# Kernel tuning notes

Hardware: AMD Instinct MI355X
Metric: run time of the kernel (lower is better)

## Reference

```python
import jax, jax.numpy as jnp
import numpy as np
import math

D = 512
L = 1024
B = 2
N_SETS = 4
PLANES = 4
POS_PLANES = 16
TOTAL_PLANES = N_SETS * PLANES


def setup_inputs() -> dict:
    key = jax.random.key(0)
    ks = jax.random.split(key, 24)
    s = 0.02
    rn = lambda k, shp: jax.random.normal(k, shp, dtype=jnp.float32) * s
    inp = {
        "x": jax.random.normal(ks[0], (B, L, D), dtype=jnp.float32),
        # key encoder: Linear(D,D) -> GELU -> Linear(D,total_planes)
        "ke_w1": rn(ks[1], (D, D)), "ke_b1": jnp.zeros((D,), jnp.float32),
        "ke_w2": rn(ks[2], (D, TOTAL_PLANES)), "ke_b2": jnp.zeros((TOTAL_PLANES,), jnp.float32),
        # query encoder
        "qe_w1": rn(ks[3], (D, D)), "qe_b1": jnp.zeros((D,), jnp.float32),
        "qe_w2": rn(ks[4], (D, TOTAL_PLANES)), "qe_b2": jnp.zeros((TOTAL_PLANES,), jnp.float32),
        # to_value
        "v_w": rn(ks[5], (D, D)), "v_b": jnp.zeros((D,), jnp.float32),
        # to_out: LayerNorm(D) then Linear(D,D)
        "ln_g": jnp.ones((D,), jnp.float32), "ln_b": jnp.zeros((D,), jnp.float32),
        "out_w": rn(ks[6], (D, D)), "out_b": jnp.zeros((D,), jnp.float32),
        # set mixing weights, positional weight
        "set_weights": jnp.ones((N_SETS,), jnp.float32),
        "pos_weight": jnp.ones((1,), jnp.float32),
        # content_pos_gate: Linear(D, D//2) -> GELU -> Linear(D//2, 1) -> Sigmoid
        "gate_w1": rn(ks[7], (D, D // 2)), "gate_b1": jnp.zeros((D // 2,), jnp.float32),
        "gate_w2": rn(ks[8], (D // 2, 1)), "gate_b2": jnp.zeros((1,), jnp.float32),
        # positional frequencies (buffer)
        "pos_freqs": jnp.exp(jnp.arange(POS_PLANES, dtype=jnp.float32) * (-math.log(10000.0) / POS_PLANES)),
    }
    return inp


def reference(x, ke_w1, ke_b1, ke_w2, ke_b2, qe_w1, qe_b1, qe_w2, qe_b2,
              v_w, v_b, ln_g, ln_b, out_w, out_b, set_weights, pos_weight,
              gate_w1, gate_b1, gate_w2, gate_b2, pos_freqs):
    b, l, d = x.shape
    n_sets = set_weights.shape[0]
    total_planes = ke_w2.shape[1]
    planes = total_planes // n_sets

    gelu = lambda t: jax.nn.gelu(t, approximate=False)  # torch default GELU is exact

    key_phase = jnp.tanh(gelu(x @ ke_w1 + ke_b1) @ ke_w2 + ke_b2) * math.pi  # [B,L,P]
    query_phase = jnp.tanh(gelu(x @ qe_w1 + qe_b1) @ qe_w2 + qe_b2) * math.pi
    V = x @ v_w + v_b  # [B,L,D]

    kp = key_phase.reshape(b, l, n_sets, planes)
    qp = query_phase.reshape(b, l, n_sets, planes)
    w = jax.nn.softmax(set_weights)

    # complex phasor outer-product cumsum in real arithmetic:
    # bound = exp(i*kp) * V ; memory = cumsum_L(bound) ; retrieved = Re(memory * exp(-i*qp))
    Vb = V[:, :, None, None, :]                                   # [B,L,1,1,D]
    cum_re = jnp.cumsum(jnp.cos(kp)[..., None] * Vb, axis=1)      # [B,L,S,p,D]
    cum_im = jnp.cumsum(jnp.sin(kp)[..., None] * Vb, axis=1)
    retrieved = (cum_re * jnp.cos(qp)[..., None] + cum_im * jnp.sin(qp)[..., None]).sum(axis=3)  # [B,L,S,D]
    total_retrieved = jnp.einsum('blsd,s->bld', retrieved, w)

    # positional plane
    pos = jnp.arange(l, dtype=jnp.float32)[:, None]
    pos_phase = pos * pos_freqs * (2.0 * math.pi)                 # [L,PP]
    cp = jnp.cos(pos_phase)[None, :, :, None]                     # [1,L,PP,1]
    sp = jnp.sin(pos_phase)[None, :, :, None]
    Vp = V[:, :, None, :]                                          # [B,L,1,D]
    cumP_re = jnp.cumsum(cp * Vp, axis=1)                          # [B,L,PP,D]
    cumP_im = jnp.cumsum(sp * Vp, axis=1)
    retrieved_pos = (cumP_re * cp + cumP_im * sp).sum(axis=2)      # [B,L,D]

    gate = jax.nn.sigmoid(gelu(x @ gate_w1 + gate_b1) @ gate_w2 + gate_b2)  # [B,L,1]
    pos_contribution = jax.nn.sigmoid(pos_weight) * retrieved_pos
    total_retrieved = gate * total_retrieved + (1.0 - gate) * pos_contribution

    positions = jnp.arange(1, l + 1, dtype=jnp.float32)
    norm = jnp.sqrt(positions * planes)[None, :, None]
    h = total_retrieved / norm

    # to_out: LayerNorm then Linear
    mu = h.mean(axis=-1, keepdims=True)
    var = ((h - mu) ** 2).mean(axis=-1, keepdims=True)
    h_ln = (h - mu) / jnp.sqrt(var + 1e-5) * ln_g + ln_b
    return x + h_ln @ out_w + out_b
```

## Files before the change

kernel.cpp:

```cpp
#include <hip/hip_runtime.h>

typedef unsigned short u16;
typedef __attribute__((ext_vector_type(8))) __bf16 bf16x8;
typedef __attribute__((ext_vector_type(4))) float f32x4;

#define DI __device__ __forceinline__

DI u16 f2b(float f){ union{float f; unsigned u;} x; x.f = f; unsigned u = x.u;
  return (u16)((u + 0x7FFFu + ((u>>16)&1u)) >> 16); }

#define NCH 16
#define CLEN 64

__global__ __launch_bounds__(256) void k_cast(const float* __restrict__ x, u16* __restrict__ xb) {
  int i = (blockIdx.x*256 + threadIdx.x)*8;
  float4 a = *(const float4*)(x+i);
  float4 b = *(const float4*)(x+i+4);
  unsigned o0 = (unsigned)f2b(a.x) | ((unsigned)f2b(a.y)<<16);
  unsigned o1 = (unsigned)f2b(a.z) | ((unsigned)f2b(a.w)<<16);
  unsigned o2 = (unsigned)f2b(b.x) | ((unsigned)f2b(b.y)<<16);
  unsigned o3 = (unsigned)f2b(b.z) | ((unsigned)f2b(b.w)<<16);
  *(uint4*)(xb+i) = make_uint4(o0,o1,o2,o3);
}

__global__ void k_transpose(const float* w0, const float* w1, const float* w2, const float* w3, const float* w4,
                            u16* t0, u16* t1, u16* t2, u16* t3, u16* t4) {
  __shared__ u16 tile[32][33];
  int z = blockIdx.z;
  const float* src; u16* dst; int K, N;
  if (z==0){src=w0;dst=t0;K=512;N=512;}
  else if(z==1){src=w1;dst=t1;K=512;N=512;}
  else if(z==2){src=w2;dst=t2;K=512;N=512;}
  else if(z==3){src=w3;dst=t3;K=512;N=256;}
  else        {src=w4;dst=t4;K=512;N=512;}
  int n0 = blockIdx.x*32, k0 = blockIdx.y*32;
  if (n0 >= N) return;
  int tx = threadIdx.x, ty = threadIdx.y;
  #pragma unroll
  for (int r = 0; r < 4; r++) tile[ty + 8*r][tx] = f2b(src[(k0 + ty + 8*r)*N + n0 + tx]);
  __syncthreads();
  #pragma unroll
  for (int r = 0; r < 4; r++) dst[(n0 + ty + 8*r)*K + k0 + tx] = tile[tx][ty + 8*r];
}

__global__ __launch_bounds__(256) void k_gemm4(const u16* __restrict__ A, const u16* __restrict__ BTF,
                       const float* __restrict__ kb1, const float* __restrict__ qb1,
                       const float* __restrict__ vb,  const float* __restrict__ gb1,
                       float* __restrict__ Hke, float* __restrict__ Hqe,
                       float* __restrict__ V,   float* __restrict__ Hg) {
  const int K = 512;
  __shared__ short As[64][48];
  __shared__ short Bs[64][48];
  int t = threadIdx.x;
  int bm = blockIdx.y*64, bn = blockIdx.x*64;
  int lane = t & 63, wid = t >> 6;
  int wm = (wid>>1)*32, wn = (wid&1)*32;
  int lr = lane & 15, ls = lane >> 4;
  f32x4 zero = {0.f,0.f,0.f,0.f};
  f32x4 acc[2][2];
  acc[0][0]=zero; acc[0][1]=zero; acc[1][0]=zero; acc[1][1]=zero;
  int srow = t >> 2, scol = (t & 3)*8;
  for (int k0 = 0; k0 < K; k0 += 32) {
    __syncthreads();
    *(bf16x8*)&As[srow][scol] = *(const bf16x8*)(A   + (bm+srow)*K + k0 + scol);
    *(bf16x8*)&Bs[srow][scol] = *(const bf16x8*)(BTF + (bn+srow)*K + k0 + scol);
    __syncthreads();
    bf16x8 a0 = *(const bf16x8*)&As[wm + lr][ls*8];
    bf16x8 a1 = *(const bf16x8*)&As[wm + 16 + lr][ls*8];
    bf16x8 b0 = *(const bf16x8*)&Bs[wn + lr][ls*8];
    bf16x8 b1 = *(const bf16x8*)&Bs[wn + 16 + lr][ls*8];
    acc[0][0] = __builtin_amdgcn_mfma_f32_16x16x32_bf16(a0, b0, acc[0][0], 0,0,0);
    acc[0][1] = __builtin_amdgcn_mfma_f32_16x16x32_bf16(a0, b1, acc[0][1], 0,0,0);
    acc[1][0] = __builtin_amdgcn_mfma_f32_16x16x32_bf16(a1, b0, acc[1][0], 0,0,0);
    acc[1][1] = __builtin_amdgcn_mfma_f32_16x16x32_bf16(a1, b1, acc[1][1], 0,0,0);
  }
  float* C; const float* bias; int nstr, nb; bool gel;
  if (bn < 512)       { C=Hke; bias=kb1; nstr=512; nb=bn;      gel=true;  }
  else if (bn < 1024) { C=Hqe; bias=qb1; nstr=512; nb=bn-512;  gel=true;  }
  else if (bn < 1536) { C=V;   bias=vb;  nstr=512; nb=bn-1024; gel=false; }
  else                { C=Hg;  bias=gb1; nstr=256; nb=bn-1536; gel=true;  }
  #pragma unroll
  for (int fm = 0; fm < 2; fm++)
    #pragma unroll
    for (int fn = 0; fn < 2; fn++)
      #pragma unroll
      for (int r = 0; r < 4; r++) {
        int grow = bm + wm + fm*16 + ls*4 + r;
        int gcol = nb + wn + fn*16 + lr;
        float v = acc[fm][fn][r] + bias[gcol];
        if (gel) v = 0.5f*v*(1.0f + erff(v*0.70710678118654752f));
        C[grow*nstr + gcol] = v;
      }
}

__global__ __launch_bounds__(256) void k_gemm_out(const u16* __restrict__ A, const u16* __restrict__ BT,
                       const float* __restrict__ bias, const float* __restrict__ resid,
                       float* __restrict__ C, int M, int N, int K) {
  __shared__ short As[64][48];
  __shared__ short Bs[64][48];
  int t = threadIdx.x;
  int bm = blockIdx.y*64, bn = blockIdx.x*64;
  int lane = t & 63, wid = t >> 6;
  int wm = (wid>>1)*32, wn = (wid&1)*32;
  int lr = lane & 15, ls = lane >> 4;
  f32x4 zero = {0.f,0.f,0.f,0.f};
  f32x4 acc[2][2];
  acc[0][0]=zero; acc[0][1]=zero; acc[1][0]=zero; acc[1][1]=zero;
  int srow = t >> 2, scol = (t & 3)*8;
  for (int k0 = 0; k0 < K; k0 += 32) {
    __syncthreads();
    *(bf16x8*)&As[srow][scol] = *(const bf16x8*)(A  + (bm+srow)*K + k0 + scol);
    *(bf16x8*)&Bs[srow][scol] = *(const bf16x8*)(BT + (bn+srow)*K + k0 + scol);
    __syncthreads();
    bf16x8 a0 = *(const bf16x8*)&As[wm + lr][ls*8];
    bf16x8 a1 = *(const bf16x8*)&As[wm + 16 + lr][ls*8];
    bf16x8 b0 = *(const bf16x8*)&Bs[wn + lr][ls*8];
    bf16x8 b1 = *(const bf16x8*)&Bs[wn + 16 + lr][ls*8];
    acc[0][0] = __builtin_amdgcn_mfma_f32_16x16x32_bf16(a0, b0, acc[0][0], 0,0,0);
    acc[0][1] = __builtin_amdgcn_mfma_f32_16x16x32_bf16(a0, b1, acc[0][1], 0,0,0);
    acc[1][0] = __builtin_amdgcn_mfma_f32_16x16x32_bf16(a1, b0, acc[1][0], 0,0,0);
    acc[1][1] = __builtin_amdgcn_mfma_f32_16x16x32_bf16(a1, b1, acc[1][1], 0,0,0);
  }
  #pragma unroll
  for (int fm = 0; fm < 2; fm++)
    #pragma unroll
    for (int fn = 0; fn < 2; fn++)
      #pragma unroll
      for (int r = 0; r < 4; r++) {
        int grow = bm + wm + fm*16 + ls*4 + r;
        int gcol = bn + wn + fn*16 + lr;
        float v = acc[fm][fn][r] + bias[gcol] + resid[grow*N + gcol];
        C[grow*N + gcol] = v;
      }
}

__global__ __launch_bounds__(256) void k_phase(const float* __restrict__ Hke, const float* __restrict__ Hqe,
                        const float* __restrict__ Hg,
                        const float* __restrict__ kw2, const float* __restrict__ kb2,
                        const float* __restrict__ qw2, const float* __restrict__ qb2,
                        const float* __restrict__ gw2, const float* __restrict__ gb2,
                        const float* __restrict__ setw, const float* __restrict__ posw,
                        const float* __restrict__ freqs,
                        float* __restrict__ ub, float* __restrict__ ab) {
  int t = threadIdx.x;
  int wid = t >> 6, lane = t & 63;
  int r = blockIdx.x*4 + wid;
  int l = r & 1023;
  int p = lane & 15, s = lane >> 4;
  const float* hk = Hke + r*512 + s*128;
  const float* hq = Hqe + r*512 + s*128;
  float kps = 0.f, qps = 0.f;
  for (int i0 = 0; i0 < 128; i0 += 4) {
    float4 hkv = *(const float4*)(hk + i0);
    float4 hqv = *(const float4*)(hq + i0);
    int kb = (s*128 + i0)*16 + p;
    kps += hkv.x * kw2[kb];      qps += hqv.x * qw2[kb];
    kps += hkv.y * kw2[kb+16];   qps += hqv.y * qw2[kb+16];
    kps += hkv.z * kw2[kb+32];   qps += hqv.z * qw2[kb+32];
    kps += hkv.w * kw2[kb+48];   qps += hqv.w * qw2[kb+48];
  }
  kps += __shfl_xor(kps, 16); kps += __shfl_xor(kps, 32);
  qps += __shfl_xor(qps, 16); qps += __shfl_xor(qps, 32);
  const float PI = 3.14159265358979323846f;
  float kph = tanhf(kps + kb2[p]) * PI;
  float qph = tanhf(qps + qb2[p]) * PI;
  const float* hg = Hg + r*256;
  float4 hgv = *(const float4*)(hg + lane*4);
  float gp = hgv.x*gw2[lane*4] + hgv.y*gw2[lane*4+1]
           + hgv.z*gw2[lane*4+2] + hgv.w*gw2[lane*4+3];
  #pragma unroll
  for (int m = 1; m <= 32; m <<= 1) gp += __shfl_xor(gp, m);
  float gate = 1.f/(1.f + expf(-(gp + gb2[0])));
  float pph = (float)l * freqs[p] * 6.2831853071795864769f;
  float s0=setw[0], s1=setw[1], s2=setw[2], s3=setw[3];
  float mx = fmaxf(fmaxf(s0,s1), fmaxf(s2,s3));
  float e0=expf(s0-mx), e1=expf(s1-mx), e2=expf(s2-mx), e3=expf(s3-mx);
  float esum = e0+e1+e2+e3;
  int si = p >> 2;
  float wsel = (si==0? e0 : si==1? e1 : si==2? e2 : e3) / esum;
  float sigpw = 1.f/(1.f + expf(-posw[0]));
  float invnorm = rsqrtf((float)(l+1) * 4.0f);
  if (lane < 16) {
    float sk, ck, sq, cq, sp, cp;
    sincosf(kph, &sk, &ck);
    sincosf(qph, &sq, &cq);
    sincosf(pph, &sp, &cp);
    float* urow = ub + r*64;
    float* arow = ab + r*64;
    urow[p]      = ck;
    urow[16 + p] = sk;
    urow[32 + p] = cp;
    urow[48 + p] = sp;
    float ga = gate * wsel * invnorm;
    float pa = (1.f - gate) * sigpw * invnorm;
    arow[p]      = ga * cq;
    arow[16 + p] = ga * sq;
    arow[32 + p] = pa * cp;
    arow[48 + p] = pa * sp;
  }
}

__global__ __launch_bounds__(256) void k_scanA(const float* __restrict__ ub, const float* __restrict__ V,
                        float* __restrict__ P) {
  __shared__ float ul[CLEN][64];
  __shared__ float vl[CLEN][64];
  int t = threadIdx.x;
  int d0 = blockIdx.x*64; int c = blockIdx.y; int b = blockIdx.z;
  int srow = t >> 2, scol = (t & 3)*16;
  {
    const float* up = ub + (b*1024 + c*CLEN + srow)*64 + scol;
    *(float4*)&ul[srow][scol]    = *(const float4*)up;
    *(float4*)&ul[srow][scol+4]  = *(const float4*)(up+4);
    *(float4*)&ul[srow][scol+8]  = *(const float4*)(up+8);
    *(float4*)&ul[srow][scol+12] = *(const float4*)(up+12);
    const float* vp = V + (b*1024 + c*CLEN + srow)*512 + d0 + scol;
    *(float4*)&vl[srow][scol]    = *(const float4*)vp;
    *(float4*)&vl[srow][scol+4]  = *(const float4*)(vp+4);
    *(float4*)&vl[srow][scol+8]  = *(const float4*)(vp+8);
    *(float4*)&vl[srow][scol+12] = *(const float4*)(vp+12);
  }
  __syncthreads();
  int dd = t & 63, kg = t >> 6;
  float acc[16];
  #pragma unroll
  for (int i=0;i<16;i++) acc[i]=0.f;
  for (int tt = 0; tt < CLEN; tt++) {
    float vv = vl[tt][dd];
    #pragma unroll
    for (int i=0;i<16;i++) acc[i] += ul[tt][kg*16+i]*vv;
  }
  float* pp = P + (((b*NCH + c)*64) + kg*16)*512 + d0 + dd;
  #pragma unroll
  for (int i=0;i<16;i++) pp[i*512] = acc[i];
}

__global__ __launch_bounds__(256) void k_scanB(float* __restrict__ P) {
  int tid = blockIdx.x*256 + threadIdx.x;
  int b = tid >> 15;
  int k = (tid >> 9) & 63;
  int d = tid & 511;
  float run = 0.f;
  float* base = P + ((b*NCH)*64 + k)*512 + d;
  for (int c = 0; c < NCH; c++) {
    float v = base[c*64*512];
    base[c*64*512] = run;
    run += v;
  }
}

__global__ __launch_bounds__(256) void k_scanC(const float* __restrict__ ub, const float* __restrict__ ab,
                        const float* __restrict__ V, const float* __restrict__ P,
                        float* __restrict__ h) {
  __shared__ float ul[CLEN][64];
  __shared__ float al[CLEN][64];
  int t = threadIdx.x;
  int c = blockIdx.y; int b = blockIdx.z;
  int srow = t >> 2, scol = (t & 3)*16;
  {
    const float* up = ub + (b*1024 + c*CLEN + srow)*64 + scol;
    *(float4*)&ul[srow][scol]    = *(const float4*)up;
    *(float4*)&ul[srow][scol+4]  = *(const float4*)(up+4);
    *(float4*)&ul[srow][scol+8]  = *(const float4*)(up+8);
    *(float4*)&ul[srow][scol+12] = *(const float4*)(up+12);
    const float* ap = ab + (b*1024 + c*CLEN + srow)*64 + scol;
    *(float4*)&al[srow][scol]    = *(const float4*)ap;
    *(float4*)&al[srow][scol+4]  = *(const float4*)(ap+4);
    *(float4*)&al[srow][scol+8]  = *(const float4*)(ap+8);
    *(float4*)&al[srow][scol+12] = *(const float4*)(ap+12);
  }
  __syncthreads();
  int kg = t & 3;
  int di = t >> 2;
  int d = blockIdx.x*64 + di;
  float s[16];
  const float* pb = P + ((b*NCH + c)*64 + kg*16)*512 + d;
  #pragma unroll
  for (int k = 0; k < 16; k++) s[k] = pb[k*512];
  const float* vrow = V + (b*1024 + c*CLEN)*512 + d;
  float* hrow = h + (b*1024 + c*CLEN)*512 + d;
  const float4* ul4 = (const float4*)&ul[0][0];
  const float4* al4 = (const float4*)&al[0][0];
  for (int tt = 0; tt < CLEN; tt++) {
    float vv = vrow[tt*512];
    float4 u0 = ul4[tt*16 + kg*4 + 0];
    float4 u1 = ul4[tt*16 + kg*4 + 1];
    float4 u2 = ul4[tt*16 + kg*4 + 2];
    float4 u3 = ul4[tt*16 + kg*4 + 3];
    float4 a0 = al4[tt*16 + kg*4 + 0];
    float4 a1 = al4[tt*16 + kg*4 + 1];
    float4 a2 = al4[tt*16 + kg*4 + 2];
    float4 a3 = al4[tt*16 + kg*4 + 3];
    float h0=0.f, h1=0.f, h2=0.f, h3=0.f;
    s[0]  += u0.x*vv; h0 += a0.x*s[0];
    s[1]  += u0.y*vv; h1 += a0.y*s[1];
    s[2]  += u0.z*vv; h2 += a0.z*s[2];
    s[3]  += u0.w*vv; h3 += a0.w*s[3];
    s[4]  += u1.x*vv; h0 += a1.x*s[4];
    s[5]  += u1.y*vv; h1 += a1.y*s[5];
    s[6]  += u1.z*vv; h2 += a1.z*s[6];
    s[7]  += u1.w*vv; h3 += a1.w*s[7];
    s[8]  += u2.x*vv; h0 += a2.x*s[8];
    s[9]  += u2.y*vv; h1 += a2.y*s[9];
    s[10] += u2.z*vv; h2 += a2.z*s[10];
    s[11] += u2.w*vv; h3 += a2.w*s[11];
    s[12] += u3.x*vv; h0 += a3.x*s[12];
    s[13] += u3.y*vv; h1 += a3.y*s[13];
    s[14] += u3.z*vv; h2 += a3.z*s[14];
    s[15] += u3.w*vv; h3 += a3.w*s[15];
    float hp = (h0+h1)+(h2+h3);
    hp += __shfl_xor(hp, 1);
    hp += __shfl_xor(hp, 2);
    if (kg == 0) hrow[tt*512] = hp;
  }
}

__global__ __launch_bounds__(256) void k_ln(const float* __restrict__ h, const float* __restrict__ g,
                     const float* __restrict__ bta, u16* __restrict__ hln) {
  int t = threadIdx.x;
  int wid = t >> 6, lane = t & 63;
  int r = blockIdx.x*4 + wid;
  const float* hr = h + r*512;
  float4 v0 = *(const float4*)(hr + lane*8);
  float4 v1 = *(const float4*)(hr + lane*8 + 4);
  float vals[8] = {v0.x,v0.y,v0.z,v0.w,v1.x,v1.y,v1.z,v1.w};
  float sum = 0.f, sq = 0.f;
  #pragma unroll
  for (int i=0;i<8;i++){ sum += vals[i]; sq += vals[i]*vals[i]; }
  #pragma unroll
  for (int m = 1; m <= 32; m <<= 1){ sum += __shfl_xor(sum, m); sq += __shfl_xor(sq, m); }
  float mu = sum * (1.f/512.f);
  float var = sq * (1.f/512.f) - mu*mu;
  float rstd = rsqrtf(var + 1e-5f);
  unsigned o[4];
  #pragma unroll
  for (int i=0;i<4;i++){
    u16 lo = f2b((vals[2*i]  -mu)*rstd*g[lane*8+2*i]   + bta[lane*8+2*i]);
    u16 hi = f2b((vals[2*i+1]-mu)*rstd*g[lane*8+2*i+1] + bta[lane*8+2*i+1]);
    o[i] = (unsigned)lo | ((unsigned)hi << 16);
  }
  uint4 ov = make_uint4(o[0],o[1],o[2],o[3]);
  *(uint4*)(hln + r*512 + lane*8) = ov;
}

extern "C" void kernel_launch(void* const* d_in, const int* in_sizes, int n_in,
                              void* d_out, int out_size, void* d_ws, size_t ws_size,
                              hipStream_t stream) {
  const float* x       = (const float*)d_in[0];
  const float* ke_w1   = (const float*)d_in[1];
  const float* ke_b1   = (const float*)d_in[2];
  const float* ke_w2   = (const float*)d_in[3];
  const float* ke_b2   = (const float*)d_in[4];
  const float* qe_w1   = (const float*)d_in[5];
  const float* qe_b1   = (const float*)d_in[6];
  const float* qe_w2   = (const float*)d_in[7];
  const float* qe_b2   = (const float*)d_in[8];
  const float* v_w     = (const float*)d_in[9];
  const float* v_b     = (const float*)d_in[10];
  const float* ln_g    = (const float*)d_in[11];
  const float* ln_b    = (const float*)d_in[12];
  const float* out_w   = (const float*)d_in[13];
  const float* out_b   = (const float*)d_in[14];
  const float* setw    = (const float*)d_in[15];
  const float* posw    = (const float*)d_in[16];
  const float* gate_w1 = (const float*)d_in[17];
  const float* gate_b1 = (const float*)d_in[18];
  const float* gate_w2 = (const float*)d_in[19];
  const float* gate_b2 = (const float*)d_in[20];
  const float* freqs   = (const float*)d_in[21];
  float* out = (float*)d_out;

  char* ws = (char*)d_ws;
  u16*   xb  = (u16*)(ws + 0);
  u16*   BTF = (u16*)(ws + 2097152);
  u16*   oT  = (u16*)(ws + 3932160);
  float* Hke = (float*)(ws + 4456448);
  float* Hqe = (float*)(ws + 8650752);
  float* Hg  = (float*)(ws + 12845056);
  float* V   = (float*)(ws + 14942208);
  float* ubf = (float*)(ws + 19136512);
  float* abf = (float*)(ws + 19660800);
  float* P   = (float*)(ws + 20185088);
  float* h   = Hke;
  u16*   hln = (u16*)Hqe;

  u16* keT = BTF;
  u16* qeT = BTF + 512*512;
  u16* vT  = BTF + 1024*512;
  u16* gT  = BTF + 1536*512;

  k_cast<<<512,256,0,stream>>>(x, xb);
  k_transpose<<<dim3(16,16,5), dim3(32,8), 0, stream>>>(ke_w1,qe_w1,v_w,gate_w1,out_w,
                                                        keT,qeT,vT,gT,oT);
  k_gemm4<<<dim3(28,32),256,0,stream>>>(xb, BTF, ke_b1, qe_b1, v_b, gate_b1,
                                        Hke, Hqe, V, Hg);
  k_phase<<<512,256,0,stream>>>(Hke,Hqe,Hg, ke_w2,ke_b2, qe_w2,qe_b2,
                                gate_w2,gate_b2, setw,posw,freqs, ubf,abf);
  k_scanA<<<dim3(8,NCH,2),256,0,stream>>>(ubf, V, P);
  k_scanB<<<256,256,0,stream>>>(P);
  k_scanC<<<dim3(8,NCH,2),256,0,stream>>>(ubf, abf, V, P, h);
  k_ln<<<512,256,0,stream>>>(h, ln_g, ln_b, hln);
  k_gemm_out<<<dim3(8,32),256,0,stream>>>(hln, oT, out_b, x, out, 2048,512,512);
}
```

Measured before the change: 85.97 us.

## Use 128x128 GEMM tiles with double-buffered direct-to-LDS loads and merge prep kernels

Both GEMM kernels move from 64x64 tiles with register-staged shared-memory copies to 128x128 tiles. Each warp now computes a 4x4 grid of MFMA fragments, and operand tiles are double-buffered and loaded straight into LDS with global_load_lds, so the next K-step loads overlap the current MFMAs. The cast and weight-transpose kernels are merged into one launch. The risks are fewer blocks than CUs for the output GEMM, bank conflicts from the unpadded LDS layout, and higher register pressure.

```diff
diff --git a/kernel.cpp b/kernel.cpp
--- a/kernel.cpp
+++ b/kernel.cpp
@@ -9,33 +9,44 @@
 DI u16 f2b(float f){ union{float f; unsigned u;} x; x.f = f; unsigned u = x.u;
   return (u16)((u + 0x7FFFu + ((u>>16)&1u)) >> 16); }
 
+DI void gload16(const void* g, void* l) {
+  __builtin_amdgcn_global_load_lds(
+      (const __attribute__((address_space(1))) void*)g,
+      (__attribute__((address_space(3))) void*)l, 16, 0, 0);
+}
+
 #define NCH 16
 #define CLEN 64
 
-__global__ __launch_bounds__(256) void k_cast(const float* __restrict__ x, u16* __restrict__ xb) {
-  int i = (blockIdx.x*256 + threadIdx.x)*8;
-  float4 a = *(const float4*)(x+i);
-  float4 b = *(const float4*)(x+i+4);
-  unsigned o0 = (unsigned)f2b(a.x) | ((unsigned)f2b(a.y)<<16);
-  unsigned o1 = (unsigned)f2b(a.z) | ((unsigned)f2b(a.w)<<16);
-  unsigned o2 = (unsigned)f2b(b.x) | ((unsigned)f2b(b.y)<<16);
-  unsigned o3 = (unsigned)f2b(b.z) | ((unsigned)f2b(b.w)<<16);
-  *(uint4*)(xb+i) = make_uint4(o0,o1,o2,o3);
-}
-
-__global__ void k_transpose(const float* w0, const float* w1, const float* w2, const float* w3, const float* w4,
+__global__ __launch_bounds__(256) void k_prep(const float* __restrict__ x, u16* __restrict__ xb,
+                            const float* w0, const float* w1, const float* w2, const float* w3, const float* w4,
                             u16* t0, u16* t1, u16* t2, u16* t3, u16* t4) {
   __shared__ u16 tile[32][33];
-  int z = blockIdx.z;
+  int z = blockIdx.x;
+  int t = threadIdx.x;
+  if (z < 512) {
+    int i = (z*256 + t)*8;
+    float4 a = *(const float4*)(x+i);
+    float4 b = *(const float4*)(x+i+4);
+    unsigned o0 = (unsigned)f2b(a.x) | ((unsigned)f2b(a.y)<<16);
+    unsigned o1 = (unsigned)f2b(a.z) | ((unsigned)f2b(a.w)<<16);
+    unsigned o2 = (unsigned)f2b(b.x) | ((unsigned)f2b(b.y)<<16);
+    unsigned o3 = (unsigned)f2b(b.z) | ((unsigned)f2b(b.w)<<16);
+    *(uint4*)(xb+i) = make_uint4(o0,o1,o2,o3);
+    return;
+  }
+  z -= 512;
+  int which = z >> 8;
+  int rem = z & 255;
   const float* src; u16* dst; int K, N;
-  if (z==0){src=w0;dst=t0;K=512;N=512;}
-  else if(z==1){src=w1;dst=t1;K=512;N=512;}
-  else if(z==2){src=w2;dst=t2;K=512;N=512;}
-  else if(z==3){src=w3;dst=t3;K=512;N=256;}
-  else        {src=w4;dst=t4;K=512;N=512;}
-  int n0 = blockIdx.x*32, k0 = blockIdx.y*32;
+  if (which==0){src=w0;dst=t0;K=512;N=512;}
+  else if(which==1){src=w1;dst=t1;K=512;N=512;}
+  else if(which==2){src=w2;dst=t2;K=512;N=512;}
+  else if(which==3){src=w3;dst=t3;K=512;N=256;}
+  else             {src=w4;dst=t4;K=512;N=512;}
+  int n0 = (rem & 15)*32, k0 = (rem >> 4)*32;
   if (n0 >= N) return;
-  int tx = threadIdx.x, ty = threadIdx.y;
+  int tx = t & 31, ty = t >> 5;
   #pragma unroll
   for (int r = 0; r < 4; r++) tile[ty + 8*r][tx] = f2b(src[(k0 + ty + 8*r)*N + n0 + tx]);
   __syncthreads();
@@ -43,51 +54,71 @@
   for (int r = 0; r < 4; r++) dst[(n0 + ty + 8*r)*K + k0 + tx] = tile[tx][ty + 8*r];
 }
 
+#define GEMM_MAINLOOP(A_, BT_, K_, bm_, bn_)                                           \
+  __shared__ short smem[2][8192];                                                      \
+  int t = threadIdx.x;                                                                 \
+  int lane = t & 63, wid = t >> 6;                                                     \
+  int lr = lane & 15, ls = lane >> 4;                                                  \
+  int wm = (wid>>1)*64, wn = (wid&1)*64;                                               \
+  f32x4 acc[4][4];                                                                     \
+  {f32x4 z_ = {0.f,0.f,0.f,0.f};                                                       \
+   _Pragma("unroll") for (int i_=0;i_<4;i_++) _Pragma("unroll") for (int j_=0;j_<4;j_++) acc[i_][j_]=z_;} \
+  int rr_ = t >> 2, cc_ = (t & 3)*8;                                                   \
+  const u16* gpa0_ = A_  + (bm_ + rr_)*K_      + cc_;                                  \
+  const u16* gpa1_ = A_  + (bm_ + 64 + rr_)*K_ + cc_;                                  \
+  const u16* gpb0_ = BT_ + (bn_ + rr_)*K_      + cc_;                                  \
+  const u16* gpb1_ = BT_ + (bn_ + 64 + rr_)*K_ + cc_;                                  \
+  int woff_ = wid*512;                                                                 \
+                                                        \
+  { short* lb_ = &smem[0][woff_];                                                      \
+    gload16(gpa0_, lb_); gload16(gpa1_, lb_+2048);                                     \
+    gload16(gpb0_, lb_+4096); gload16(gpb1_, lb_+6144); }                              \
+  __syncthreads();                                                                     \
+  const int NSTEP_ = (K_)/32;                                                          \
+  for (int st_ = 0; st_ < NSTEP_; st_++) {                                             \
+    int buf_ = st_ & 1;                                                                \
+    if (st_ + 1 < NSTEP_) {                                                            \
+      int kk_ = (st_+1)*32;                                                            \
+      short* lb_ = &smem[buf_^1][woff_];                                               \
+      gload16(gpa0_+kk_, lb_); gload16(gpa1_+kk_, lb_+2048);                           \
+      gload16(gpb0_+kk_, lb_+4096); gload16(gpb1_+kk_, lb_+6144);                      \
+    }                                                                                  \
+    bf16x8 afr_[4], bfr_[4];                                                           \
+    _Pragma("unroll")                                                                  \
+    for (int mi = 0; mi < 4; mi++)                                                     \
+      afr_[mi] = *(const bf16x8*)&smem[buf_][(wm + mi*16 + lr)*32 + ls*8];             \
+    _Pragma("unroll")                                                                  \
+    for (int ni = 0; ni < 4; ni++)                                                     \
+      bfr_[ni] = *(const bf16x8*)&smem[buf_][4096 + (wn + ni*16 + lr)*32 + ls*8];      \
+    _Pragma("unroll")                                                                  \
+    for (int mi = 0; mi < 4; mi++)                                                     \
+      _Pragma("unroll")                                                                \
+      for (int ni = 0; ni < 4; ni++)                                                   \
+        acc[mi][ni] = __builtin_amdgcn_mfma_f32_16x16x32_bf16(afr_[mi], bfr_[ni], acc[mi][ni], 0,0,0); \
+    __syncthreads();                                                                   \
+  }
+
 __global__ __launch_bounds__(256) void k_gemm4(const u16* __restrict__ A, const u16* __restrict__ BTF,
                        const float* __restrict__ kb1, const float* __restrict__ qb1,
-                       const float* __restrict__ vb,  const float* __restrict__ gb1,
+                       const float* __restrict__ vb,  const float* __restrict__ gbias1,
                        float* __restrict__ Hke, float* __restrict__ Hqe,
                        float* __restrict__ V,   float* __restrict__ Hg) {
-  const int K = 512;
-  __shared__ short As[64][48];
-  __shared__ short Bs[64][48];
-  int t = threadIdx.x;
-  int bm = blockIdx.y*64, bn = blockIdx.x*64;
-  int lane = t & 63, wid = t >> 6;
-  int wm = (wid>>1)*32, wn = (wid&1)*32;
-  int lr = lane & 15, ls = lane >> 4;
-  f32x4 zero = {0.f,0.f,0.f,0.f};
-  f32x4 acc[2][2];
-  acc[0][0]=zero; acc[0][1]=zero; acc[1][0]=zero; acc[1][1]=zero;
-  int srow = t >> 2, scol = (t & 3)*8;
-  for (int k0 = 0; k0 < K; k0 += 32) {
-    __syncthreads();
-    *(bf16x8*)&As[srow][scol] = *(const bf16x8*)(A   + (bm+srow)*K + k0 + scol);
-    *(bf16x8*)&Bs[srow][scol] = *(const bf16x8*)(BTF + (bn+srow)*K + k0 + scol);
-    __syncthreads();
-    bf16x8 a0 = *(const bf16x8*)&As[wm + lr][ls*8];
-    bf16x8 a1 = *(const bf16x8*)&As[wm + 16 + lr][ls*8];
-    bf16x8 b0 = *(const bf16x8*)&Bs[wn + lr][ls*8];
-    bf16x8 b1 = *(const bf16x8*)&Bs[wn + 16 + lr][ls*8];
-    acc[0][0] = __builtin_amdgcn_mfma_f32_16x16x32_bf16(a0, b0, acc[0][0], 0,0,0);
-    acc[0][1] = __builtin_amdgcn_mfma_f32_16x16x32_bf16(a0, b1, acc[0][1], 0,0,0);
-    acc[1][0] = __builtin_amdgcn_mfma_f32_16x16x32_bf16(a1, b0, acc[1][0], 0,0,0);
-    acc[1][1] = __builtin_amdgcn_mfma_f32_16x16x32_bf16(a1, b1, acc[1][1], 0,0,0);
-  }
+  int bm = blockIdx.y*128, bn = blockIdx.x*128;
+  GEMM_MAINLOOP(A, BTF, 512, bm, bn)
   float* C; const float* bias; int nstr, nb; bool gel;
-  if (bn < 512)       { C=Hke; bias=kb1; nstr=512; nb=bn;      gel=true;  }
-  else if (bn < 1024) { C=Hqe; bias=qb1; nstr=512; nb=bn-512;  gel=true;  }
-  else if (bn < 1536) { C=V;   bias=vb;  nstr=512; nb=bn-1024; gel=false; }
-  else                { C=Hg;  bias=gb1; nstr=256; nb=bn-1536; gel=true;  }
-  #pragma unroll
-  for (int fm = 0; fm < 2; fm++)
+  if (bn < 512)       { C=Hke; bias=kb1;    nstr=512; nb=bn;      gel=true;  }
+  else if (bn < 1024) { C=Hqe; bias=qb1;    nstr=512; nb=bn-512;  gel=true;  }
+  else if (bn < 1536) { C=V;   bias=vb;     nstr=512; nb=bn-1024; gel=false; }
+  else                { C=Hg;  bias=gbias1; nstr=256; nb=bn-1536; gel=true;  }
+  #pragma unroll
+  for (int mi = 0; mi < 4; mi++)
     #pragma unroll
-    for (int fn = 0; fn < 2; fn++)
+    for (int ni = 0; ni < 4; ni++)
       #pragma unroll
       for (int r = 0; r < 4; r++) {
-        int grow = bm + wm + fm*16 + ls*4 + r;
-        int gcol = nb + wn + fn*16 + lr;
-        float v = acc[fm][fn][r] + bias[gcol];
+        int grow = bm + wm + mi*16 + ls*4 + r;
+        int gcol = nb + wn + ni*16 + lr;
+        float v = acc[mi][ni][r] + bias[gcol];
         if (gel) v = 0.5f*v*(1.0f + erff(v*0.70710678118654752f));
         C[grow*nstr + gcol] = v;
       }
@@ -95,42 +126,19 @@
 
 __global__ __launch_bounds__(256) void k_gemm_out(const u16* __restrict__ A, const u16* __restrict__ BT,
                        const float* __restrict__ bias, const float* __restrict__ resid,
-                       float* __restrict__ C, int M, int N, int K) {
-  __shared__ short As[64][48];
-  __shared__ short Bs[64][48];
-  int t = threadIdx.x;
-  int bm = blockIdx.y*64, bn = blockIdx.x*64;
-  int lane = t & 63, wid = t >> 6;
-  int wm = (wid>>1)*32, wn = (wid&1)*32;
-  int lr = lane & 15, ls = lane >> 4;
-  f32x4 zero = {0.f,0.f,0.f,0.f};
-  f32x4 acc[2][2];
-  acc[0][0]=zero; acc[0][1]=zero; acc[1][0]=zero; acc[1][1]=zero;
-  int srow = t >> 2, scol = (t & 3)*8;
-  for (int k0 = 0; k0 < K; k0 += 32) {
-    __syncthreads();
-    *(bf16x8*)&As[srow][scol] = *(const bf16x8*)(A  + (bm+srow)*K + k0 + scol);
-    *(bf16x8*)&Bs[srow][scol] = *(const bf16x8*)(BT + (bn+srow)*K + k0 + scol);
-    __syncthreads();
-    bf16x8 a0 = *(const bf16x8*)&As[wm + lr][ls*8];
-    bf16x8 a1 = *(const bf16x8*)&As[wm + 16 + lr][ls*8];
-    bf16x8 b0 = *(const bf16x8*)&Bs[wn + lr][ls*8];
-    bf16x8 b1 = *(const bf16x8*)&Bs[wn + 16 + lr][ls*8];
-    acc[0][0] = __builtin_amdgcn_mfma_f32_16x16x32_bf16(a0, b0, acc[0][0], 0,0,0);
-    acc[0][1] = __builtin_amdgcn_mfma_f32_16x16x32_bf16(a0, b1, acc[0][1], 0,0,0);
-    acc[1][0] = __builtin_amdgcn_mfma_f32_16x16x32_bf16(a1, b0, acc[1][0], 0,0,0);
-    acc[1][1] = __builtin_amdgcn_mfma_f32_16x16x32_bf16(a1, b1, acc[1][1], 0,0,0);
-  }
-  #pragma unroll
-  for (int fm = 0; fm < 2; fm++)
+                       float* __restrict__ C) {
+  int bm = blockIdx.y*128, bn = blockIdx.x*128;
+  GEMM_MAINLOOP(A, BT, 512, bm, bn)
+  #pragma unroll
+  for (int mi = 0; mi < 4; mi++)
     #pragma unroll
-    for (int fn = 0; fn < 2; fn++)
+    for (int ni = 0; ni < 4; ni++)
       #pragma unroll
       for (int r = 0; r < 4; r++) {
-        int grow = bm + wm + fm*16 + ls*4 + r;
-        int gcol = bn + wn + fn*16 + lr;
-        float v = acc[fm][fn][r] + bias[gcol] + resid[grow*N + gcol];
-        C[grow*N + gcol] = v;
+        int grow = bm + wm + mi*16 + ls*4 + r;
+        int gcol = bn + wn + ni*16 + lr;
+        float v = acc[mi][ni][r] + bias[gcol] + resid[grow*512 + gcol];
+        C[grow*512 + gcol] = v;
       }
 }
 
@@ -388,10 +396,9 @@
   u16* vT  = BTF + 1024*512;
   u16* gT  = BTF + 1536*512;
 
-  k_cast<<<512,256,0,stream>>>(x, xb);
-  k_transpose<<<dim3(16,16,5), dim3(32,8), 0, stream>>>(ke_w1,qe_w1,v_w,gate_w1,out_w,
-                                                        keT,qeT,vT,gT,oT);
-  k_gemm4<<<dim3(28,32),256,0,stream>>>(xb, BTF, ke_b1, qe_b1, v_b, gate_b1,
+  k_prep<<<512 + 5*256, 256, 0, stream>>>(x, xb, ke_w1,qe_w1,v_w,gate_w1,out_w,
+                                          keT,qeT,vT,gT,oT);
+  k_gemm4<<<dim3(14,16),256,0,stream>>>(xb, BTF, ke_b1, qe_b1, v_b, gate_b1,
                                         Hke, Hqe, V, Hg);
   k_phase<<<512,256,0,stream>>>(Hke,Hqe,Hg, ke_w2,ke_b2, qe_w2,qe_b2,
                                 gate_w2,gate_b2, setw,posw,freqs, ubf,abf);
@@ -399,5 +406,5 @@
   k_scanB<<<256,256,0,stream>>>(P);
   k_scanC<<<dim3(8,NCH,2),256,0,stream>>>(ubf, abf, V, P, h);
   k_ln<<<512,256,0,stream>>>(h, ln_g, ln_b, hln);
-  k_gemm_out<<<dim3(8,32),256,0,stream>>>(hln, oT, out_b, x, out, 2048,512,512);
-}
+  k_gemm_out<<<dim3(4,16),256,0,stream>>>(hln, oT, out_b, x, out);
+}
```

New measurement: 102.1 us. 1.19x slower.

## Fuse cast/transpose, merge scan carry into scanC, fold LayerNorm into output GEMM

Applied to the files above, without the earlier changes.

Merges the input cast and weight transpose into one prep kernel. Removes the separate chunk-carry scan kernel: each scanC block now sums the partial states of all earlier chunks itself. Removes the LayerNorm kernel by computing row statistics inside the output GEMM and normalizing and casting to bf16 while staging the A tile. This cuts four launches and the intermediate bf16 buffer, at the cost of redundant prefix summation and repeated LN statistic reads across column blocks.

```diff
diff --git a/kernel.cpp b/kernel.cpp
--- a/kernel.cpp
+++ b/kernel.cpp
@@ -12,30 +12,35 @@
 #define NCH 16
 #define CLEN 64
 
-__global__ __launch_bounds__(256) void k_cast(const float* __restrict__ x, u16* __restrict__ xb) {
-  int i = (blockIdx.x*256 + threadIdx.x)*8;
-  float4 a = *(const float4*)(x+i);
-  float4 b = *(const float4*)(x+i+4);
-  unsigned o0 = (unsigned)f2b(a.x) | ((unsigned)f2b(a.y)<<16);
-  unsigned o1 = (unsigned)f2b(a.z) | ((unsigned)f2b(a.w)<<16);
-  unsigned o2 = (unsigned)f2b(b.x) | ((unsigned)f2b(b.y)<<16);
-  unsigned o3 = (unsigned)f2b(b.z) | ((unsigned)f2b(b.w)<<16);
-  *(uint4*)(xb+i) = make_uint4(o0,o1,o2,o3);
-}
-
-__global__ void k_transpose(const float* w0, const float* w1, const float* w2, const float* w3, const float* w4,
+__global__ __launch_bounds__(256) void k_prep(const float* __restrict__ x, u16* __restrict__ xb,
+                            const float* w0, const float* w1, const float* w2, const float* w3, const float* w4,
                             u16* t0, u16* t1, u16* t2, u16* t3, u16* t4) {
   __shared__ u16 tile[32][33];
-  int z = blockIdx.z;
+  int z = blockIdx.x;
+  int t = threadIdx.x;
+  if (z < 512) {
+    int i = (z*256 + t)*8;
+    float4 a = *(const float4*)(x+i);
+    float4 b = *(const float4*)(x+i+4);
+    unsigned o0 = (unsigned)f2b(a.x) | ((unsigned)f2b(a.y)<<16);
+    unsigned o1 = (unsigned)f2b(a.z) | ((unsigned)f2b(a.w)<<16);
+    unsigned o2 = (unsigned)f2b(b.x) | ((unsigned)f2b(b.y)<<16);
+    unsigned o3 = (unsigned)f2b(b.z) | ((unsigned)f2b(b.w)<<16);
+    *(uint4*)(xb+i) = make_uint4(o0,o1,o2,o3);
+    return;
+  }
+  z -= 512;
+  int which = z >> 8;
+  int rem = z & 255;
   const float* src; u16* dst; int K, N;
-  if (z==0){src=w0;dst=t0;K=512;N=512;}
-  else if(z==1){src=w1;dst=t1;K=512;N=512;}
-  else if(z==2){src=w2;dst=t2;K=512;N=512;}
-  else if(z==3){src=w3;dst=t3;K=512;N=256;}
-  else        {src=w4;dst=t4;K=512;N=512;}
-  int n0 = blockIdx.x*32, k0 = blockIdx.y*32;
+  if (which==0){src=w0;dst=t0;K=512;N=512;}
+  else if(which==1){src=w1;dst=t1;K=512;N=512;}
+  else if(which==2){src=w2;dst=t2;K=512;N=512;}
+  else if(which==3){src=w3;dst=t3;K=512;N=256;}
+  else             {src=w4;dst=t4;K=512;N=512;}
+  int n0 = (rem & 15)*32, k0 = (rem >> 4)*32;
   if (n0 >= N) return;
-  int tx = threadIdx.x, ty = threadIdx.y;
+  int tx = t & 31, ty = t >> 5;
   #pragma unroll
   for (int r = 0; r < 4; r++) tile[ty + 8*r][tx] = f2b(src[(k0 + ty + 8*r)*N + n0 + tx]);
   __syncthreads();
@@ -45,7 +50,7 @@
 
 __global__ __launch_bounds__(256) void k_gemm4(const u16* __restrict__ A, const u16* __restrict__ BTF,
                        const float* __restrict__ kb1, const float* __restrict__ qb1,
-                       const float* __restrict__ vb,  const float* __restrict__ gb1,
+                       const float* __restrict__ vb,  const float* __restrict__ gbias1,
                        float* __restrict__ Hke, float* __restrict__ Hqe,
                        float* __restrict__ V,   float* __restrict__ Hg) {
   const int K = 512;
@@ -75,10 +80,10 @@
     acc[1][1] = __builtin_amdgcn_mfma_f32_16x16x32_bf16(a1, b1, acc[1][1], 0,0,0);
   }
   float* C; const float* bias; int nstr, nb; bool gel;
-  if (bn < 512)       { C=Hke; bias=kb1; nstr=512; nb=bn;      gel=true;  }
-  else if (bn < 1024) { C=Hqe; bias=qb1; nstr=512; nb=bn-512;  gel=true;  }
-  else if (bn < 1536) { C=V;   bias=vb;  nstr=512; nb=bn-1024; gel=false; }
-  else                { C=Hg;  bias=gb1; nstr=256; nb=bn-1536; gel=true;  }
+  if (bn < 512)       { C=Hke; bias=kb1;    nstr=512; nb=bn;      gel=true;  }
+  else if (bn < 1024) { C=Hqe; bias=qb1;    nstr=512; nb=bn-512;  gel=true;  }
+  else if (bn < 1536) { C=V;   bias=vb;     nstr=512; nb=bn-1024; gel=false; }
+  else                { C=Hg;  bias=gbias1; nstr=256; nb=bn-1536; gel=true;  }
   #pragma unroll
   for (int fm = 0; fm < 2; fm++)
     #pragma unroll
@@ -93,23 +98,61 @@
       }
 }
 
-__global__ __launch_bounds__(256) void k_gemm_out(const u16* __restrict__ A, const u16* __restrict__ BT,
+__global__ __launch_bounds__(256) void k_gemm_out_ln(
+                       const float* __restrict__ h,   const float* __restrict__ lng,
+                       const float* __restrict__ lnb, const u16* __restrict__ BT,
                        const float* __restrict__ bias, const float* __restrict__ resid,
-                       float* __restrict__ C, int M, int N, int K) {
+                       float* __restrict__ C) {
+  const int K = 512;
   __shared__ short As[64][48];
   __shared__ short Bs[64][48];
+  __shared__ float mu_s[64], rs_s[64];
   int t = threadIdx.x;
   int bm = blockIdx.y*64, bn = blockIdx.x*64;
   int lane = t & 63, wid = t >> 6;
   int wm = (wid>>1)*32, wn = (wid&1)*32;
   int lr = lane & 15, ls = lane >> 4;
+  {
+    int r = t >> 2, q = t & 3;
+    const float* hr = h + (bm + r)*512 + q*128;
+    float sum = 0.f, sq = 0.f;
+    #pragma unroll 8
+    for (int i = 0; i < 128; i += 4) {
+      float4 v = *(const float4*)(hr + i);
+      sum += (v.x+v.y)+(v.z+v.w);
+      sq  += (v.x*v.x+v.y*v.y)+(v.z*v.z+v.w*v.w);
+    }
+    sum += __shfl_xor(sum,1); sum += __shfl_xor(sum,2);
+    sq  += __shfl_xor(sq,1);  sq  += __shfl_xor(sq,2);
+    if (q == 0) {
+      float mu = sum * (1.f/512.f);
+      float var = sq * (1.f/512.f) - mu*mu;
+      mu_s[r] = mu;
+      rs_s[r] = rsqrtf(var + 1e-5f);
+    }
+  }
+  __syncthreads();
   f32x4 zero = {0.f,0.f,0.f,0.f};
   f32x4 acc[2][2];
   acc[0][0]=zero; acc[0][1]=zero; acc[1][0]=zero; acc[1][1]=zero;
   int srow = t >> 2, scol = (t & 3)*8;
   for (int k0 = 0; k0 < K; k0 += 32) {
     __syncthreads();
-    *(bf16x8*)&As[srow][scol] = *(const bf16x8*)(A  + (bm+srow)*K + k0 + scol);
+    {
+      const float* hp = h + (bm+srow)*512 + k0 + scol;
+      float4 a  = *(const float4*)hp;
+      float4 b  = *(const float4*)(hp+4);
+      float4 g0 = *(const float4*)(lng + k0 + scol);
+      float4 g1 = *(const float4*)(lng + k0 + scol + 4);
+      float4 c0 = *(const float4*)(lnb + k0 + scol);
+      float4 c1 = *(const float4*)(lnb + k0 + scol + 4);
+      float mu = mu_s[srow], rs = rs_s[srow];
+      unsigned o0 = (unsigned)f2b((a.x-mu)*rs*g0.x+c0.x) | ((unsigned)f2b((a.y-mu)*rs*g0.y+c0.y)<<16);
+      unsigned o1 = (unsigned)f2b((a.z-mu)*rs*g0.z+c0.z) | ((unsigned)f2b((a.w-mu)*rs*g0.w+c0.w)<<16);
+      unsigned o2 = (unsigned)f2b((b.x-mu)*rs*g1.x+c1.x) | ((unsigned)f2b((b.y-mu)*rs*g1.y+c1.y)<<16);
+      unsigned o3 = (unsigned)f2b((b.z-mu)*rs*g1.z+c1.z) | ((unsigned)f2b((b.w-mu)*rs*g1.w+c1.w)<<16);
+      *(uint4*)&As[srow][scol] = make_uint4(o0,o1,o2,o3);
+    }
     *(bf16x8*)&Bs[srow][scol] = *(const bf16x8*)(BT + (bn+srow)*K + k0 + scol);
     __syncthreads();
     bf16x8 a0 = *(const bf16x8*)&As[wm + lr][ls*8];
@@ -129,8 +172,8 @@
       for (int r = 0; r < 4; r++) {
         int grow = bm + wm + fm*16 + ls*4 + r;
         int gcol = bn + wn + fn*16 + lr;
-        float v = acc[fm][fn][r] + bias[gcol] + resid[grow*N + gcol];
-        C[grow*N + gcol] = v;
+        float v = acc[fm][fn][r] + bias[gcol] + resid[grow*512 + gcol];
+        C[grow*512 + gcol] = v;
       }
 }
 
@@ -234,21 +277,7 @@
   for (int i=0;i<16;i++) pp[i*512] = acc[i];
 }
 
-__global__ __launch_bounds__(256) void k_scanB(float* __restrict__ P) {
-  int tid = blockIdx.x*256 + threadIdx.x;
-  int b = tid >> 15;
-  int k = (tid >> 9) & 63;
-  int d = tid & 511;
-  float run = 0.f;
-  float* base = P + ((b*NCH)*64 + k)*512 + d;
-  for (int c = 0; c < NCH; c++) {
-    float v = base[c*64*512];
-    base[c*64*512] = run;
-    run += v;
-  }
-}
-
-__global__ __launch_bounds__(256) void k_scanC(const float* __restrict__ ub, const float* __restrict__ ab,
+__global__ __launch_bounds__(256) void k_scanBC(const float* __restrict__ ub, const float* __restrict__ ab,
                         const float* __restrict__ V, const float* __restrict__ P,
                         float* __restrict__ h) {
   __shared__ float ul[CLEN][64];
@@ -273,9 +302,13 @@
   int di = t >> 2;
   int d = blockIdx.x*64 + di;
   float s[16];
-  const float* pb = P + ((b*NCH + c)*64 + kg*16)*512 + d;
-  #pragma unroll
-  for (int k = 0; k < 16; k++) s[k] = pb[k*512];
+  #pragma unroll
+  for (int k = 0; k < 16; k++) s[k] = 0.f;
+  const float* pb = P + ((b*NCH)*64 + kg*16)*512 + d;
+  for (int cc = 0; cc < c; cc++) {
+    #pragma unroll
+    for (int k = 0; k < 16; k++) s[k] += pb[(cc*64 + k)*512];
+  }
   const float* vrow = V + (b*1024 + c*CLEN)*512 + d;
   float* hrow = h + (b*1024 + c*CLEN)*512 + d;
   const float4* ul4 = (const float4*)&ul[0][0];
@@ -314,34 +347,6 @@
   }
 }
 
-__global__ __launch_bounds__(256) void k_ln(const float* __restrict__ h, const float* __restrict__ g,
-                     const float* __restrict__ bta, u16* __restrict__ hln) {
-  int t = threadIdx.x;
-  int wid = t >> 6, lane = t & 63;
-  int r = blockIdx.x*4 + wid;
-  const float* hr = h + r*512;
-  float4 v0 = *(const float4*)(hr + lane*8);
-  float4 v1 = *(const float4*)(hr + lane*8 + 4);
-  float vals[8] = {v0.x,v0.y,v0.z,v0.w,v1.x,v1.y,v1.z,v1.w};
-  float sum = 0.f, sq = 0.f;
-  #pragma unroll
-  for (int i=0;i<8;i++){ sum += vals[i]; sq += vals[i]*vals[i]; }
-  #pragma unroll
-  for (int m = 1; m <= 32; m <<= 1){ sum += __shfl_xor(sum, m); sq += __shfl_xor(sq, m); }
-  float mu = sum * (1.f/512.f);
-  float var = sq * (1.f/512.f) - mu*mu;
-  float rstd = rsqrtf(var + 1e-5f);
-  unsigned o[4];
-  #pragma unroll
-  for (int i=0;i<4;i++){
-    u16 lo = f2b((vals[2*i]  -mu)*rstd*g[lane*8+2*i]   + bta[lane*8+2*i]);
-    u16 hi = f2b((vals[2*i+1]-mu)*rstd*g[lane*8+2*i+1] + bta[lane*8+2*i+1]);
-    o[i] = (unsigned)lo | ((unsigned)hi << 16);
-  }
-  uint4 ov = make_uint4(o[0],o[1],o[2],o[3]);
-  *(uint4*)(hln + r*512 + lane*8) = ov;
-}
-
 extern "C" void kernel_launch(void* const* d_in, const int* in_sizes, int n_in,
                               void* d_out, int out_size, void* d_ws, size_t ws_size,
                               hipStream_t stream) {
@@ -381,23 +386,19 @@
   float* abf = (float*)(ws + 19660800);
   float* P   = (float*)(ws + 20185088);
   float* h   = Hke;
-  u16*   hln = (u16*)Hqe;
 
   u16* keT = BTF;
   u16* qeT = BTF + 512*512;
   u16* vT  = BTF + 1024*512;
   u16* gT  = BTF + 1536*512;
 
-  k_cast<<<512,256,0,stream>>>(x, xb);
-  k_transpose<<<dim3(16,16,5), dim3(32,8), 0, stream>>>(ke_w1,qe_w1,v_w,gate_w1,out_w,
-                                                        keT,qeT,vT,gT,oT);
+  k_prep<<<512 + 5*256, 256, 0, stream>>>(x, xb, ke_w1,qe_w1,v_w,gate_w1,out_w,
+                                          keT,qeT,vT,gT,oT);
   k_gemm4<<<dim3(28,32),256,0,stream>>>(xb, BTF, ke_b1, qe_b1, v_b, gate_b1,
                                         Hke, Hqe, V, Hg);
   k_phase<<<512,256,0,stream>>>(Hke,Hqe,Hg, ke_w2,ke_b2, qe_w2,qe_b2,
                                 gate_w2,gate_b2, setw,posw,freqs, ubf,abf);
   k_scanA<<<dim3(8,NCH,2),256,0,stream>>>(ubf, V, P);
-  k_scanB<<<256,256,0,stream>>>(P);
-  k_scanC<<<dim3(8,NCH,2),256,0,stream>>>(ubf, abf, V, P, h);
-  k_ln<<<512,256,0,stream>>>(h, ln_g, ln_b, hln);
-  k_gemm_out<<<dim3(8,32),256,0,stream>>>(hln, oT, out_b, x, out, 2048,512,512);
-}
+  k_scanBC<<<dim3(8,NCH,2),256,0,stream>>>(ubf, abf, V, P, h);
+  k_gemm_out_ln<<<dim3(8,32),256,0,stream>>>(h, ln_g, ln_b, oT, out_b, x, out);
+}
```

After: 92.67 us. 1.08x slower.
